# Performance work log

Measured on AMD Instinct MI355X. Metric: run time of the kernel, lower is better.

The kernel has to match this reference:

```python
import jax, jax.numpy as jnp
import numpy as np

B, S, E, H, Dh = 2, 2048, 1024, 16, 64


def setup_inputs() -> dict:
    key = jax.random.key(0)
    ks = jax.random.split(key, 8)
    w = 0.02
    return {
        "x": jax.random.normal(ks[0], (B, S, E), jnp.float32),
        # torch Linear convention: weight (out, in) = (Dh, E), stacked over heads
        "Wq": jax.random.normal(ks[1], (H, Dh, E), jnp.float32) * w,
        "bq": jax.random.normal(ks[2], (H, Dh), jnp.float32) * w,
        "Wk": jax.random.normal(ks[3], (H, Dh, E), jnp.float32) * w,
        "bk": jax.random.normal(ks[4], (H, Dh), jnp.float32) * w,
        "Wv": jax.random.normal(ks[5], (H, Dh, E), jnp.float32) * w,
        "bv": jax.random.normal(ks[6], (H, Dh), jnp.float32) * w,
        "proj": jax.random.normal(ks[7], (H * Dh, E), jnp.float32) * w,
    }


def reference(x, Wq, bq, Wk, bk, Wv, bv, proj):
    b, s, e = x.shape
    h, dh, _ = Wq.shape
    scale = jnp.sqrt(jnp.asarray(dh, x.dtype))
    # per-head linear projections: y = x @ W.T + b  -> (b, h, s, dh)
    q = jnp.einsum('bse,hde->bhsd', x, Wq) + bq[None, :, None, :]
    k = jnp.einsum('bse,hde->bhsd', x, Wk) + bk[None, :, None, :]
    v = jnp.einsum('bse,hde->bhsd', x, Wv) + bv[None, :, None, :]
    causal = jnp.triu(jnp.ones((s, s), bool), 1)
    scores = jnp.einsum('bhsd,bhtd->bhst', q, k) / scale
    scores = jnp.where(causal[None, None], -jnp.inf, scores)
    # quirk: softmax output divided by sqrt(head_size) a second time
    att = jax.nn.softmax(scores, axis=-1) / scale
    z = jnp.einsum('bhst,bhtd->bhsd', att, v)
    # quirk: torch reshapes (B,H,S,Dh) row-major into (B,S,H*Dh) WITHOUT transpose
    z = z.reshape(b, s, h * dh)
    return z @ proj
```

## Files before the change

kernel.cpp:

```cpp
#include <hip/hip_runtime.h>
#include <hip/hip_bf16.h>

typedef unsigned short u16;
typedef unsigned int u32;
typedef __bf16 bf16x8 __attribute__((ext_vector_type(8)));
typedef float f32x4 __attribute__((ext_vector_type(4)));
typedef u16 u16x8 __attribute__((ext_vector_type(8)));
typedef u16 u16x4 __attribute__((ext_vector_type(4)));
typedef u32 u32x4 __attribute__((ext_vector_type(4)));

#define B_ 2
#define S_ 2048
#define E_ 1024
#define H_ 16
#define Dh_ 64

static __device__ __forceinline__ u16 f2bf(float f) {
  unsigned u = __builtin_bit_cast(unsigned, f);
  u += 0x7fff + ((u >> 16) & 1);
  return (u16)(u >> 16);
}

static __device__ __forceinline__ void gload16(const u16* g, u16* l) {
  __builtin_amdgcn_global_load_lds((const __attribute__((address_space(1))) unsigned int*)g,
                                   (__attribute__((address_space(3))) unsigned int*)l,
                                   16, 0, 0);
}

__global__ void cvt_all(const float* __restrict__ x, const float* __restrict__ wq,
                        const float* __restrict__ wk, const float* __restrict__ wv,
                        u16* __restrict__ xb, u16* __restrict__ wcat) {
  const int i = blockIdx.x * 256 + threadIdx.x;
  const float* src; u16x8* dst;
  if (i < 524288) {
    src = x + (size_t)i * 8;            dst = (u16x8*)xb + i;
  } else {
    const int j = i - 524288;
    dst = (u16x8*)wcat + j;
    if (j < 131072)      src = wq + (size_t)j * 8;
    else if (j < 262144) src = wk + (size_t)(j - 131072) * 8;
    else                 src = wv + (size_t)(j - 262144) * 8;
  }
  float4 a = ((const float4*)src)[0], b = ((const float4*)src)[1];
  u16x8 o;
  o[0] = f2bf(a.x); o[1] = f2bf(a.y); o[2] = f2bf(a.z); o[3] = f2bf(a.w);
  o[4] = f2bf(b.x); o[5] = f2bf(b.y); o[6] = f2bf(b.z); o[7] = f2bf(b.w);
  *dst = o;
}

__global__ void transpose_cvt(const float* __restrict__ in, u16* __restrict__ outT) {
  __shared__ float t[32][33];
  const int e = blockIdx.x * 32 + threadIdx.x;
  const int f = blockIdx.y * 32 + threadIdx.y;
  t[threadIdx.y][threadIdx.x] = in[f * 1024 + e];
  __syncthreads();
  const int eo = blockIdx.x * 32 + threadIdx.y;
  const int fo = blockIdx.y * 32 + threadIdx.x;
  outT[eo * 1024 + fo] = f2bf(t[threadIdx.x][threadIdx.y]);
}

__global__ __launch_bounds__(256) void qkv_gemm(const u16* __restrict__ Wcat,
                                                const u16* __restrict__ Xm,
                                                const float* __restrict__ bq,
                                                const float* __restrict__ bk,
                                                const float* __restrict__ bv,
                                                u16* __restrict__ Qb, u16* __restrict__ Kb,
                                                u16* __restrict__ Vtb, float qs) {
  __shared__ __align__(16) u16 As[2][4096];
  __shared__ __align__(16) u16 Bs[2][4096];
  const int tid = threadIdx.x;
  const int wv = tid >> 6, ln = tid & 63;
  const int lq = ln & 15, lg = ln >> 4;
  const int bid = blockIdx.x;
  const int xcd = bid & 7, within = bid >> 3;
  const int bx = (xcd & 1) * 12 + within % 12;
  const int by = (xcd >> 1) * 8 + within / 12;
  const int ra0 = bx * 128, rb0 = by * 128;
  const int wra = wv >> 1, wrb = wv & 1;

  f32x4 acc[4][4];
  const f32x4 z4 = {0.f, 0.f, 0.f, 0.f};
#pragma unroll
  for (int i = 0; i < 4; ++i)
#pragma unroll
    for (int j = 0; j < 4; ++j) acc[i][j] = z4;

  const int arow = tid >> 2;
  const int acol = (tid & 3) * 8;
  const u16* Ags = Wcat + (ra0 + arow) * 1024 + acol;
  const u16* Bgs = Xm + (rb0 + arow) * 1024 + acol;

#define GSTAGE(KT, BUF) do { const int k0_ = (KT) * 32;              \
    gload16(Ags + k0_,         &As[BUF][wv * 512]);                  \
    gload16(Ags + 65536 + k0_, &As[BUF][wv * 512 + 2048]);           \
    gload16(Bgs + k0_,         &Bs[BUF][wv * 512]);                  \
    gload16(Bgs + 65536 + k0_, &Bs[BUF][wv * 512 + 2048]); } while (0)

  GSTAGE(0, 0);
  for (int kt = 0; kt < 32; ++kt) {
    const int cb = kt & 1;
    if (kt < 31) {
      GSTAGE(kt + 1, cb ^ 1);
      asm volatile("s_waitcnt vmcnt(4)" ::: "memory");
    } else {
      asm volatile("s_waitcnt vmcnt(0)" ::: "memory");
    }
    __builtin_amdgcn_s_barrier();
    __builtin_amdgcn_sched_barrier(0);
    bf16x8 af[4], bfr[4];
#pragma unroll
    for (int i = 0; i < 4; ++i)
      af[i] = *(const bf16x8*)&As[cb][(wra * 64 + i * 16 + lq) * 32 + lg * 8];
#pragma unroll
    for (int j = 0; j < 4; ++j)
      bfr[j] = *(const bf16x8*)&Bs[cb][(wrb * 64 + j * 16 + lq) * 32 + lg * 8];
#pragma unroll
    for (int i = 0; i < 4; ++i)
#pragma unroll
      for (int j = 0; j < 4; ++j)
        acc[i][j] = __builtin_amdgcn_mfma_f32_16x16x32_bf16(af[i], bfr[j], acc[i][j], 0, 0, 0);
    __builtin_amdgcn_sched_barrier(0);
    __builtin_amdgcn_s_barrier();
  }
#undef GSTAGE

  const int region = bx >> 3;
  const float* bias = (region == 0) ? bq : (region == 1) ? bk : bv;
  const float osc = (region == 0) ? qs : 1.0f;
  const int Ar = ra0 + wra * 64, Br = rb0 + wrb * 64;
#pragma unroll
  for (int i = 0; i < 4; ++i) {
#pragma unroll
    for (int j = 0; j < 4; ++j) {
      const int n0 = Ar + i * 16 + lg * 4;
      const int nl = n0 & 1023;
      const int h = nl >> 6, d = nl & 63;
      const int m = Br + j * 16 + lq;
      const int bb = m >> 11, s = m & 2047;
      const float4 b4 = *(const float4*)&bias[nl];
      if (region < 2) {
        u16* out = (region == 0) ? Qb : Kb;
        u16x4 pk;
        pk[0] = f2bf((acc[i][j][0] + b4.x) * osc);
        pk[1] = f2bf((acc[i][j][1] + b4.y) * osc);
        pk[2] = f2bf((acc[i][j][2] + b4.z) * osc);
        pk[3] = f2bf((acc[i][j][3] + b4.w) * osc);
        *(u16x4*)&out[((bb * H_ + h) * S_ + s) * Dh_ + d] = pk;
      } else {
        const float bvv[4] = {b4.x, b4.y, b4.z, b4.w};
#pragma unroll
        for (int r = 0; r < 4; ++r)
          Vtb[((bb * H_ + h) * Dh_ + d + r) * S_ + s] = f2bf(acc[i][j][r] + bvv[r]);
      }
    }
  }
}

__global__ __launch_bounds__(256) void proj_gemm(const u16* __restrict__ Am,
                                                 const u16* __restrict__ Bm,
                                                 float* __restrict__ out) {
  __shared__ __align__(16) u16 As[2][4096];
  __shared__ __align__(16) u16 Bs[2][2048];
  const int tid = threadIdx.x;
  const int wv = tid >> 6, ln = tid & 63;
  const int lq = ln & 15, lg = ln >> 4;
  const int bid = blockIdx.x;
  const int xcd = bid & 7, within = bid >> 3;
  const int bx = within & 7;
  const int by = xcd * 8 + (within >> 3);
  const int ra0 = bx * 128, rb0 = by * 64;
  const int wra = wv >> 1, wrb = wv & 1;

  f32x4 acc[4][2];
  const f32x4 z4 = {0.f, 0.f, 0.f, 0.f};
#pragma unroll
  for (int i = 0; i < 4; ++i)
#pragma unroll
    for (int j = 0; j < 2; ++j) acc[i][j] = z4;

  const int arow = tid >> 2;
  const int acol = (tid & 3) * 8;
  const int brow = wv * 16 + (ln >> 2);
  const int bcol = (ln & 3) * 8;
  const u16* Ags = Am + (ra0 + arow) * 1024 + acol;
  const u16* Bgs = Bm + (rb0 + brow) * 1024 + bcol;

#define PSTAGE(KT, BUF) do { const int k0_ = (KT) * 32;              \
    gload16(Ags + k0_,         &As[BUF][wv * 512]);                  \
    gload16(Ags + 65536 + k0_, &As[BUF][wv * 512 + 2048]);           \
    gload16(Bgs + k0_,         &Bs[BUF][wv * 512]); } while (0)

  PSTAGE(0, 0);
  for (int kt = 0; kt < 32; ++kt) {
    const int cb = kt & 1;
    if (kt < 31) {
      PSTAGE(kt + 1, cb ^ 1);
      asm volatile("s_waitcnt vmcnt(3)" ::: "memory");
    } else {
      asm volatile("s_waitcnt vmcnt(0)" ::: "memory");
    }
    __builtin_amdgcn_s_barrier();
    __builtin_amdgcn_sched_barrier(0);
    bf16x8 af[4], bfr[2];
#pragma unroll
    for (int i = 0; i < 4; ++i)
      af[i] = *(const bf16x8*)&As[cb][(wra * 64 + i * 16 + lq) * 32 + lg * 8];
#pragma unroll
    for (int j = 0; j < 2; ++j)
      bfr[j] = *(const bf16x8*)&Bs[cb][(wrb * 32 + j * 16 + lq) * 32 + lg * 8];
#pragma unroll
    for (int i = 0; i < 4; ++i)
#pragma unroll
      for (int j = 0; j < 2; ++j)
        acc[i][j] = __builtin_amdgcn_mfma_f32_16x16x32_bf16(af[i], bfr[j], acc[i][j], 0, 0, 0);
    __builtin_amdgcn_sched_barrier(0);
    __builtin_amdgcn_s_barrier();
  }
#undef PSTAGE

  const int Ar = ra0 + wra * 64, Br = rb0 + wrb * 32;
#pragma unroll
  for (int i = 0; i < 4; ++i)
#pragma unroll
    for (int j = 0; j < 2; ++j) {
      const int e0 = Ar + i * 16 + lg * 4;
      const int m = Br + j * 16 + lq;
      *(f32x4*)&out[m * 1024 + e0] = acc[i][j];
    }
}

__global__ __launch_bounds__(256) void attn_kernel(const u16* __restrict__ Q,
                                                   const u16* __restrict__ K,
                                                   const u16* __restrict__ Vt,
                                                   u16* __restrict__ Z) {
  __shared__ __align__(16) u16 Ktile[2][8192];
  __shared__ __align__(16) u16 Vtile[2][8192];
  const int tid = threadIdx.x;
  const int wv = tid >> 6, ln = tid & 63;
  const int lq = ln & 15, lg = ln >> 4;
  const bool lgodd = (lg & 1) != 0;
  const int id = blockIdx.x;
  const int within = id >> 3;
  const int xg = id & 7;
  int bh, qt;
  if (within < 32) { bh = xg * 4 + (within >> 4);     qt = 15 - (within & 15); }
  else { const int w = within - 32; bh = xg * 4 + 2 + (w >> 4); qt = w & 15; }
  const int qbase = (qt << 7) + wv * 32;
  const u16* Qp = Q + (size_t)bh * S_ * Dh_;
  const u16* Kp = K + (size_t)bh * S_ * Dh_;
  const u16* Vp = Vt + (size_t)bh * Dh_ * S_;

  int kgofs[4], vgrow[4], vgcol[4];
#pragma unroll
  for (int j = 0; j < 4; ++j) {
    const int p = wv * 256 + j * 64 + ln;
    const int gk = p ^ ((p >> 3) & 7);
    kgofs[j] = (gk >> 3) * 64 + (gk & 7) * 8;
    vgrow[j] = p >> 4;
    vgcol[j] = ((p & 15) ^ ((p >> 4) & 15)) * 8;
  }
  const int wv2 = wv * 2048;
  const int sc0 = (lg ^ (lq & 7)) * 8;
  const int sc1 = ((4 + lg) ^ (lq & 7)) * 8;

  bf16x8 qf[2][2];
#pragma unroll
  for (int m = 0; m < 2; ++m)
#pragma unroll
    for (int kk = 0; kk < 2; ++kk)
      qf[m][kk] = *(const bf16x8*)&Qp[(qbase + m * 16 + lq) * Dh_ + kk * 32 + lg * 8];

  f32x4 o[2][4];
  const f32x4 z4 = {0.f, 0.f, 0.f, 0.f};
#pragma unroll
  for (int m = 0; m < 2; ++m)
#pragma unroll
    for (int dt = 0; dt < 4; ++dt) o[m][dt] = z4;
  float l_lane[2] = {0.f, 0.f};

#define STAGE(KT, BUF) do { const int kb_ = (KT) * 128;                          \
    gload16(Kp + (size_t)kb_ * 64 + kgofs[0], &Ktile[BUF][wv2]);                 \
    gload16(Kp + (size_t)kb_ * 64 + kgofs[1], &Ktile[BUF][wv2 + 512]);           \
    gload16(Kp + (size_t)kb_ * 64 + kgofs[2], &Ktile[BUF][wv2 + 1024]);          \
    gload16(Kp + (size_t)kb_ * 64 + kgofs[3], &Ktile[BUF][wv2 + 1536]);          \
    gload16(Vp + (size_t)vgrow[0] * 2048 + kb_ + vgcol[0], &Vtile[BUF][wv2]);    \
    gload16(Vp + (size_t)vgrow[1] * 2048 + kb_ + vgcol[1], &Vtile[BUF][wv2 + 512]); \
    gload16(Vp + (size_t)vgrow[2] * 2048 + kb_ + vgcol[2], &Vtile[BUF][wv2 + 1024]); \
    gload16(Vp + (size_t)vgrow[3] * 2048 + kb_ + vgcol[3], &Vtile[BUF][wv2 + 1536]); \
  } while (0)

  STAGE(0, 0);
  __syncthreads();

  int cur = 0;
  for (int kt = 0; kt <= qt; ++kt) {
    if (kt < qt) STAGE(kt + 1, cur ^ 1);
    const int k0 = kt * 128;
    const bool diag = (kt == qt);
#pragma unroll
    for (int kk = 0; kk < 4; ++kk) {
      const int rA = (kk * 32 + lq) * 64;
      const int rB = rA + 1024;
      bf16x8 kA0 = *(const bf16x8*)&Ktile[cur][rA + sc0];
      bf16x8 kA1 = *(const bf16x8*)&Ktile[cur][rA + sc1];
      bf16x8 kB0 = *(const bf16x8*)&Ktile[cur][rB + sc0];
      bf16x8 kB1 = *(const bf16x8*)&Ktile[cur][rB + sc1];
      f32x4 sa0 = z4, sa1 = z4, sb0 = z4, sb1 = z4;
      __builtin_amdgcn_s_setprio(1);
      sa0 = __builtin_amdgcn_mfma_f32_16x16x32_bf16(kA0, qf[0][0], sa0, 0, 0, 0);
      sa0 = __builtin_amdgcn_mfma_f32_16x16x32_bf16(kA1, qf[0][1], sa0, 0, 0, 0);
      sa1 = __builtin_amdgcn_mfma_f32_16x16x32_bf16(kA0, qf[1][0], sa1, 0, 0, 0);
      sa1 = __builtin_amdgcn_mfma_f32_16x16x32_bf16(kA1, qf[1][1], sa1, 0, 0, 0);
      sb0 = __builtin_amdgcn_mfma_f32_16x16x32_bf16(kB0, qf[0][0], sb0, 0, 0, 0);
      sb0 = __builtin_amdgcn_mfma_f32_16x16x32_bf16(kB1, qf[0][1], sb0, 0, 0, 0);
      sb1 = __builtin_amdgcn_mfma_f32_16x16x32_bf16(kB0, qf[1][0], sb1, 0, 0, 0);
      sb1 = __builtin_amdgcn_mfma_f32_16x16x32_bf16(kB1, qf[1][1], sb1, 0, 0, 0);
      __builtin_amdgcn_s_setprio(0);
      if (diag) {
        const int keyA = k0 + kk * 32 + lg * 4;
        const int keyB = keyA + 16;
        const int qi0 = qbase + lq, qi1 = qbase + 16 + lq;
#pragma unroll
        for (int r = 0; r < 4; ++r) {
          if (keyA + r > qi0) sa0[r] = -3.0e38f;
          if (keyA + r > qi1) sa1[r] = -3.0e38f;
          if (keyB + r > qi0) sb0[r] = -3.0e38f;
          if (keyB + r > qi1) sb1[r] = -3.0e38f;
        }
      }
      u32 pA0[2], pA1[2], pB0[2], pB1[2];
#pragma unroll
      for (int m = 0; m < 2; ++m) {
        const f32x4 xa = m ? sa1 : sa0;
        const f32x4 xb = m ? sb1 : sb0;
        float e0 = __builtin_amdgcn_exp2f(xa[0]);
        float e1 = __builtin_amdgcn_exp2f(xa[1]);
        float e2 = __builtin_amdgcn_exp2f(xa[2]);
        float e3 = __builtin_amdgcn_exp2f(xa[3]);
        float f0 = __builtin_amdgcn_exp2f(xb[0]);
        float f1 = __builtin_amdgcn_exp2f(xb[1]);
        float f2 = __builtin_amdgcn_exp2f(xb[2]);
        float f3 = __builtin_amdgcn_exp2f(xb[3]);
        l_lane[m] += ((e0 + e1) + (e2 + e3)) + ((f0 + f1) + (f2 + f3));
        asm("v_cvt_pk_bf16_f32 %0, %1, %2" : "=v"(pA0[m]) : "v"(e0), "v"(e1));
        asm("v_cvt_pk_bf16_f32 %0, %1, %2" : "=v"(pA1[m]) : "v"(e2), "v"(e3));
        asm("v_cvt_pk_bf16_f32 %0, %1, %2" : "=v"(pB0[m]) : "v"(f0), "v"(f1));
        asm("v_cvt_pk_bf16_f32 %0, %1, %2" : "=v"(pB1[m]) : "v"(f2), "v"(f3));
      }
      bf16x8 pf[2];
#pragma unroll
      for (int m = 0; m < 2; ++m) {
        u32 A0 = pA0[m], B0 = pB0[m], A1 = pA1[m], B1 = pB1[m];
        asm("v_permlane32_swap_b32 %0, %1" : "+v"(A0), "+v"(B0));
        asm("v_permlane32_swap_b32 %0, %1" : "+v"(A1), "+v"(B1));
        const u32 A0x = __shfl_xor((int)A0, 16), B0x = __shfl_xor((int)B0, 16);
        const u32 A1x = __shfl_xor((int)A1, 16), B1x = __shfl_xor((int)B1, 16);
        u32x4 w;
        w[0] = lgodd ? B0x : A0;
        w[1] = lgodd ? B1x : A1;
        w[2] = lgodd ? B0 : A0x;
        w[3] = lgodd ? B1 : A1x;
        pf[m] = __builtin_bit_cast(bf16x8, w);
      }
      const int scvk = ((kk * 4 + lg) ^ lq) * 8;
      __builtin_amdgcn_s_setprio(1);
#pragma unroll
      for (int dt = 0; dt < 4; ++dt) {
        bf16x8 vf = *(const bf16x8*)&Vtile[cur][(dt * 16 + lq) * 128 + scvk];
        o[0][dt] = __builtin_amdgcn_mfma_f32_16x16x32_bf16(vf, pf[0], o[0][dt], 0, 0, 0);
        o[1][dt] = __builtin_amdgcn_mfma_f32_16x16x32_bf16(vf, pf[1], o[1][dt], 0, 0, 0);
      }
      __builtin_amdgcn_s_setprio(0);
    }
    if (kt < qt) {
      __syncthreads();
      cur ^= 1;
    }
  }
#undef STAGE

#pragma unroll
  for (int m = 0; m < 2; ++m) {
    float l = l_lane[m];
    l += __shfl_xor(l, 16);
    l += __shfl_xor(l, 32);
    const float inv = 0.125f / l;
    const int q_idx = qbase + m * 16 + lq;
#pragma unroll
    for (int dt = 0; dt < 4; ++dt) {
      u16x4 pko;
#pragma unroll
      for (int r = 0; r < 4; ++r) pko[r] = f2bf(o[m][dt][r] * inv);
      *(u16x4*)&Z[((size_t)bh * S_ + q_idx) * Dh_ + dt * 16 + lg * 4] = pko;
    }
  }
}

extern "C" void kernel_launch(void* const* d_in, const int* in_sizes, int n_in,
                              void* d_out, int out_size, void* d_ws, size_t ws_size,
                              hipStream_t stream) {
  const float* x    = (const float*)d_in[0];
  const float* Wq   = (const float*)d_in[1];
  const float* bq   = (const float*)d_in[2];
  const float* Wk   = (const float*)d_in[3];
  const float* bk   = (const float*)d_in[4];
  const float* Wv   = (const float*)d_in[5];
  const float* bv   = (const float*)d_in[6];
  const float* proj = (const float*)d_in[7];
  float* out = (float*)d_out;

  char* p = (char*)d_ws;
  u16* xb   = (u16*)p; p += (size_t)4096 * 1024 * 2;
  u16* wcat = (u16*)p; p += (size_t)3072 * 1024 * 2;
  u16* pjt  = (u16*)p; p += (size_t)1024 * 1024 * 2;
  u16* Qb   = (u16*)p; p += (size_t)4096 * 1024 * 2;
  u16* Kb   = (u16*)p; p += (size_t)4096 * 1024 * 2;
  u16* Vtb  = (u16*)p; p += (size_t)4096 * 1024 * 2;
  u16* Zb   = (u16*)p; p += (size_t)4096 * 1024 * 2;

  cvt_all<<<dim3(3584), dim3(256), 0, stream>>>(x, Wq, Wk, Wv, xb, wcat);
  transpose_cvt<<<dim3(32, 32), dim3(32, 32), 0, stream>>>(proj, pjt);

  const float qs = 0.125f * 1.44269504f;
  qkv_gemm<<<dim3(768), dim3(256), 0, stream>>>(wcat, xb, bq, bk, bv, Qb, Kb, Vtb, qs);

  attn_kernel<<<dim3(512), dim3(256), 0, stream>>>(Qb, Kb, Vtb, Zb);

  proj_gemm<<<dim3(512), dim3(256), 0, stream>>>(pjt, Zb, out);
}
```

Baseline: 113.6 us.

## Halve attention tiles, skip masked diagonal chunks, triple-buffer GEMM pipelines

The attention kernel now uses 64-query by 64-key tiles with 16 queries per wave, and launches twice as many blocks. On the diagonal tile it skips key chunks that are fully masked for a wave. The aim is better load balance and occupancy, plus less wasted causal work. Both GEMMs move from double to triple buffering of their LDS stages, prefetching two k-tiles ahead to hide more load latency. The trade-off is more LDS per GEMM block and more K/V reloads per query in attention, since each block now covers fewer queries.

```diff
diff --git a/kernel.cpp b/kernel.cpp
--- a/kernel.cpp
+++ b/kernel.cpp
@@ -66,8 +66,8 @@
                                                 const float* __restrict__ bv,
                                                 u16* __restrict__ Qb, u16* __restrict__ Kb,
                                                 u16* __restrict__ Vtb, float qs) {
-  __shared__ __align__(16) u16 As[2][4096];
-  __shared__ __align__(16) u16 Bs[2][4096];
+  __shared__ __align__(16) u16 As[3][4096];
+  __shared__ __align__(16) u16 Bs[3][4096];
   const int tid = threadIdx.x;
   const int wv = tid >> 6, ln = tid & 63;
   const int lq = ln & 15, lg = ln >> 4;
@@ -97,10 +97,13 @@
     gload16(Bgs + 65536 + k0_, &Bs[BUF][wv * 512 + 2048]); } while (0)
 
   GSTAGE(0, 0);
+  GSTAGE(1, 1);
   for (int kt = 0; kt < 32; ++kt) {
-    const int cb = kt & 1;
-    if (kt < 31) {
-      GSTAGE(kt + 1, cb ^ 1);
+    const int cb = kt % 3;
+    if (kt < 30) {
+      GSTAGE(kt + 2, (kt + 2) % 3);
+      asm volatile("s_waitcnt vmcnt(8)" ::: "memory");
+    } else if (kt == 30) {
       asm volatile("s_waitcnt vmcnt(4)" ::: "memory");
     } else {
       asm volatile("s_waitcnt vmcnt(0)" ::: "memory");
@@ -159,8 +162,8 @@
 __global__ __launch_bounds__(256) void proj_gemm(const u16* __restrict__ Am,
                                                  const u16* __restrict__ Bm,
                                                  float* __restrict__ out) {
-  __shared__ __align__(16) u16 As[2][4096];
-  __shared__ __align__(16) u16 Bs[2][2048];
+  __shared__ __align__(16) u16 As[3][4096];
+  __shared__ __align__(16) u16 Bs[3][2048];
   const int tid = threadIdx.x;
   const int wv = tid >> 6, ln = tid & 63;
   const int lq = ln & 15, lg = ln >> 4;
@@ -191,10 +194,13 @@
     gload16(Bgs + k0_,         &Bs[BUF][wv * 512]); } while (0)
 
   PSTAGE(0, 0);
+  PSTAGE(1, 1);
   for (int kt = 0; kt < 32; ++kt) {
-    const int cb = kt & 1;
-    if (kt < 31) {
-      PSTAGE(kt + 1, cb ^ 1);
+    const int cb = kt % 3;
+    if (kt < 30) {
+      PSTAGE(kt + 2, (kt + 2) % 3);
+      asm volatile("s_waitcnt vmcnt(6)" ::: "memory");
+    } else if (kt == 30) {
       asm volatile("s_waitcnt vmcnt(3)" ::: "memory");
     } else {
       asm volatile("s_waitcnt vmcnt(0)" ::: "memory");
@@ -233,60 +239,48 @@
                                                    const u16* __restrict__ K,
                                                    const u16* __restrict__ Vt,
                                                    u16* __restrict__ Z) {
-  __shared__ __align__(16) u16 Ktile[2][8192];
-  __shared__ __align__(16) u16 Vtile[2][8192];
+  __shared__ __align__(16) u16 Ktile[2][4096];
+  __shared__ __align__(16) u16 Vtile[2][4096];
   const int tid = threadIdx.x;
   const int wv = tid >> 6, ln = tid & 63;
   const int lq = ln & 15, lg = ln >> 4;
   const bool lgodd = (lg & 1) != 0;
   const int id = blockIdx.x;
+  const int xg = id & 7;
   const int within = id >> 3;
-  const int xg = id & 7;
-  int bh, qt;
-  if (within < 32) { bh = xg * 4 + (within >> 4);     qt = 15 - (within & 15); }
-  else { const int w = within - 32; bh = xg * 4 + 2 + (w >> 4); qt = w & 15; }
-  const int qbase = (qt << 7) + wv * 32;
+  const int grp = within >> 5;
+  const int w2 = within & 31;
+  const int bh = xg * 4 + grp;
+  const int qt = (grp & 1) ? w2 : (31 - w2);
+  const int qbase = qt * 64 + wv * 16;
+  const int q_idx = qbase + lq;
   const u16* Qp = Q + (size_t)bh * S_ * Dh_;
   const u16* Kp = K + (size_t)bh * S_ * Dh_;
   const u16* Vp = Vt + (size_t)bh * Dh_ * S_;
 
-  int kgofs[4], vgrow[4], vgcol[4];
-#pragma unroll
-  for (int j = 0; j < 4; ++j) {
-    const int p = wv * 256 + j * 64 + ln;
-    const int gk = p ^ ((p >> 3) & 7);
-    kgofs[j] = (gk >> 3) * 64 + (gk & 7) * 8;
-    vgrow[j] = p >> 4;
-    vgcol[j] = ((p & 15) ^ ((p >> 4) & 15)) * 8;
-  }
-  const int wv2 = wv * 2048;
+  const int p0 = wv * 128 + ln, p1 = p0 + 64;
+  const int g0 = p0 ^ ((p0 >> 3) & 7), g1 = p1 ^ ((p1 >> 3) & 7);
+  const int gr0 = g0 >> 3, gc0 = (g0 & 7) * 8;
+  const int gr1 = g1 >> 3, gc1 = (g1 & 7) * 8;
+  const int lb0 = wv * 1024, lb1 = wv * 1024 + 512;
   const int sc0 = (lg ^ (lq & 7)) * 8;
   const int sc1 = ((4 + lg) ^ (lq & 7)) * 8;
 
-  bf16x8 qf[2][2];
-#pragma unroll
-  for (int m = 0; m < 2; ++m)
-#pragma unroll
-    for (int kk = 0; kk < 2; ++kk)
-      qf[m][kk] = *(const bf16x8*)&Qp[(qbase + m * 16 + lq) * Dh_ + kk * 32 + lg * 8];
-
-  f32x4 o[2][4];
+  bf16x8 qf[2];
+  qf[0] = *(const bf16x8*)&Qp[q_idx * Dh_ + lg * 8];
+  qf[1] = *(const bf16x8*)&Qp[q_idx * Dh_ + 32 + lg * 8];
+
+  f32x4 o[4];
   const f32x4 z4 = {0.f, 0.f, 0.f, 0.f};
 #pragma unroll
-  for (int m = 0; m < 2; ++m)
-#pragma unroll
-    for (int dt = 0; dt < 4; ++dt) o[m][dt] = z4;
-  float l_lane[2] = {0.f, 0.f};
-
-#define STAGE(KT, BUF) do { const int kb_ = (KT) * 128;                          \
-    gload16(Kp + (size_t)kb_ * 64 + kgofs[0], &Ktile[BUF][wv2]);                 \
-    gload16(Kp + (size_t)kb_ * 64 + kgofs[1], &Ktile[BUF][wv2 + 512]);           \
-    gload16(Kp + (size_t)kb_ * 64 + kgofs[2], &Ktile[BUF][wv2 + 1024]);          \
-    gload16(Kp + (size_t)kb_ * 64 + kgofs[3], &Ktile[BUF][wv2 + 1536]);          \
-    gload16(Vp + (size_t)vgrow[0] * 2048 + kb_ + vgcol[0], &Vtile[BUF][wv2]);    \
-    gload16(Vp + (size_t)vgrow[1] * 2048 + kb_ + vgcol[1], &Vtile[BUF][wv2 + 512]); \
-    gload16(Vp + (size_t)vgrow[2] * 2048 + kb_ + vgcol[2], &Vtile[BUF][wv2 + 1024]); \
-    gload16(Vp + (size_t)vgrow[3] * 2048 + kb_ + vgcol[3], &Vtile[BUF][wv2 + 1536]); \
+  for (int dt = 0; dt < 4; ++dt) o[dt] = z4;
+  float l_lane = 0.f;
+
+#define STAGE(KT, BUF) do { const int kb_ = (KT) * 64;                       \
+    gload16(Kp + (size_t)(kb_ + gr0) * 64 + gc0, &Ktile[BUF][lb0]);          \
+    gload16(Kp + (size_t)(kb_ + gr1) * 64 + gc1, &Ktile[BUF][lb1]);          \
+    gload16(Vp + (size_t)gr0 * 2048 + kb_ + gc0, &Vtile[BUF][lb0]);          \
+    gload16(Vp + (size_t)gr1 * 2048 + kb_ + gc1, &Vtile[BUF][lb1]);          \
   } while (0)
 
   STAGE(0, 0);
@@ -295,62 +289,48 @@
   int cur = 0;
   for (int kt = 0; kt <= qt; ++kt) {
     if (kt < qt) STAGE(kt + 1, cur ^ 1);
-    const int k0 = kt * 128;
+    const int k0 = kt * 64;
     const bool diag = (kt == qt);
-#pragma unroll
-    for (int kk = 0; kk < 4; ++kk) {
-      const int rA = (kk * 32 + lq) * 64;
-      const int rB = rA + 1024;
-      bf16x8 kA0 = *(const bf16x8*)&Ktile[cur][rA + sc0];
-      bf16x8 kA1 = *(const bf16x8*)&Ktile[cur][rA + sc1];
-      bf16x8 kB0 = *(const bf16x8*)&Ktile[cur][rB + sc0];
-      bf16x8 kB1 = *(const bf16x8*)&Ktile[cur][rB + sc1];
-      f32x4 sa0 = z4, sa1 = z4, sb0 = z4, sb1 = z4;
-      __builtin_amdgcn_s_setprio(1);
-      sa0 = __builtin_amdgcn_mfma_f32_16x16x32_bf16(kA0, qf[0][0], sa0, 0, 0, 0);
-      sa0 = __builtin_amdgcn_mfma_f32_16x16x32_bf16(kA1, qf[0][1], sa0, 0, 0, 0);
-      sa1 = __builtin_amdgcn_mfma_f32_16x16x32_bf16(kA0, qf[1][0], sa1, 0, 0, 0);
-      sa1 = __builtin_amdgcn_mfma_f32_16x16x32_bf16(kA1, qf[1][1], sa1, 0, 0, 0);
-      sb0 = __builtin_amdgcn_mfma_f32_16x16x32_bf16(kB0, qf[0][0], sb0, 0, 0, 0);
-      sb0 = __builtin_amdgcn_mfma_f32_16x16x32_bf16(kB1, qf[0][1], sb0, 0, 0, 0);
-      sb1 = __builtin_amdgcn_mfma_f32_16x16x32_bf16(kB0, qf[1][0], sb1, 0, 0, 0);
-      sb1 = __builtin_amdgcn_mfma_f32_16x16x32_bf16(kB1, qf[1][1], sb1, 0, 0, 0);
-      __builtin_amdgcn_s_setprio(0);
-      if (diag) {
-        const int keyA = k0 + kk * 32 + lg * 4;
-        const int keyB = keyA + 16;
-        const int qi0 = qbase + lq, qi1 = qbase + 16 + lq;
-#pragma unroll
-        for (int r = 0; r < 4; ++r) {
-          if (keyA + r > qi0) sa0[r] = -3.0e38f;
-          if (keyA + r > qi1) sa1[r] = -3.0e38f;
-          if (keyB + r > qi0) sb0[r] = -3.0e38f;
-          if (keyB + r > qi1) sb1[r] = -3.0e38f;
+    const int nkk = diag ? ((wv >> 1) + 1) : 2;
+#pragma unroll
+    for (int kk = 0; kk < 2; ++kk) {
+      if (kk < nkk) {
+        const int rA = (kk * 32 + lq) * 64;
+        const int rB = rA + 1024;
+        bf16x8 kA0 = *(const bf16x8*)&Ktile[cur][rA + sc0];
+        bf16x8 kA1 = *(const bf16x8*)&Ktile[cur][rA + sc1];
+        bf16x8 kB0 = *(const bf16x8*)&Ktile[cur][rB + sc0];
+        bf16x8 kB1 = *(const bf16x8*)&Ktile[cur][rB + sc1];
+        f32x4 sa = z4, sb = z4;
+        __builtin_amdgcn_s_setprio(1);
+        sa = __builtin_amdgcn_mfma_f32_16x16x32_bf16(kA0, qf[0], sa, 0, 0, 0);
+        sa = __builtin_amdgcn_mfma_f32_16x16x32_bf16(kA1, qf[1], sa, 0, 0, 0);
+        sb = __builtin_amdgcn_mfma_f32_16x16x32_bf16(kB0, qf[0], sb, 0, 0, 0);
+        sb = __builtin_amdgcn_mfma_f32_16x16x32_bf16(kB1, qf[1], sb, 0, 0, 0);
+        __builtin_amdgcn_s_setprio(0);
+        if (diag) {
+          const int keyA = k0 + kk * 32 + lg * 4;
+          const int keyB = keyA + 16;
+#pragma unroll
+          for (int r = 0; r < 4; ++r) {
+            if (keyA + r > q_idx) sa[r] = -3.0e38f;
+            if (keyB + r > q_idx) sb[r] = -3.0e38f;
+          }
         }
-      }
-      u32 pA0[2], pA1[2], pB0[2], pB1[2];
-#pragma unroll
-      for (int m = 0; m < 2; ++m) {
-        const f32x4 xa = m ? sa1 : sa0;
-        const f32x4 xb = m ? sb1 : sb0;
-        float e0 = __builtin_amdgcn_exp2f(xa[0]);
-        float e1 = __builtin_amdgcn_exp2f(xa[1]);
-        float e2 = __builtin_amdgcn_exp2f(xa[2]);
-        float e3 = __builtin_amdgcn_exp2f(xa[3]);
-        float f0 = __builtin_amdgcn_exp2f(xb[0]);
-        float f1 = __builtin_amdgcn_exp2f(xb[1]);
-        float f2 = __builtin_amdgcn_exp2f(xb[2]);
-        float f3 = __builtin_amdgcn_exp2f(xb[3]);
-        l_lane[m] += ((e0 + e1) + (e2 + e3)) + ((f0 + f1) + (f2 + f3));
-        asm("v_cvt_pk_bf16_f32 %0, %1, %2" : "=v"(pA0[m]) : "v"(e0), "v"(e1));
-        asm("v_cvt_pk_bf16_f32 %0, %1, %2" : "=v"(pA1[m]) : "v"(e2), "v"(e3));
-        asm("v_cvt_pk_bf16_f32 %0, %1, %2" : "=v"(pB0[m]) : "v"(f0), "v"(f1));
-        asm("v_cvt_pk_bf16_f32 %0, %1, %2" : "=v"(pB1[m]) : "v"(f2), "v"(f3));
-      }
-      bf16x8 pf[2];
-#pragma unroll
-      for (int m = 0; m < 2; ++m) {
-        u32 A0 = pA0[m], B0 = pB0[m], A1 = pA1[m], B1 = pB1[m];
+        float e0 = __builtin_amdgcn_exp2f(sa[0]);
+        float e1 = __builtin_amdgcn_exp2f(sa[1]);
+        float e2 = __builtin_amdgcn_exp2f(sa[2]);
+        float e3 = __builtin_amdgcn_exp2f(sa[3]);
+        float f0 = __builtin_amdgcn_exp2f(sb[0]);
+        float f1 = __builtin_amdgcn_exp2f(sb[1]);
+        float f2 = __builtin_amdgcn_exp2f(sb[2]);
+        float f3 = __builtin_amdgcn_exp2f(sb[3]);
+        l_lane += ((e0 + e1) + (e2 + e3)) + ((f0 + f1) + (f2 + f3));
+        u32 A0, A1, B0, B1;
+        asm("v_cvt_pk_bf16_f32 %0, %1, %2" : "=v"(A0) : "v"(e0), "v"(e1));
+        asm("v_cvt_pk_bf16_f32 %0, %1, %2" : "=v"(A1) : "v"(e2), "v"(e3));
+        asm("v_cvt_pk_bf16_f32 %0, %1, %2" : "=v"(B0) : "v"(f0), "v"(f1));
+        asm("v_cvt_pk_bf16_f32 %0, %1, %2" : "=v"(B1) : "v"(f2), "v"(f3));
         asm("v_permlane32_swap_b32 %0, %1" : "+v"(A0), "+v"(B0));
         asm("v_permlane32_swap_b32 %0, %1" : "+v"(A1), "+v"(B1));
         const u32 A0x = __shfl_xor((int)A0, 16), B0x = __shfl_xor((int)B0, 16);
@@ -360,17 +340,16 @@
         w[1] = lgodd ? B1x : A1;
         w[2] = lgodd ? B0 : A0x;
         w[3] = lgodd ? B1 : A1x;
-        pf[m] = __builtin_bit_cast(bf16x8, w);
+        const bf16x8 pf = __builtin_bit_cast(bf16x8, w);
+        const int scvk = ((kk * 4 + lg) ^ (lq & 7)) * 8;
+        __builtin_amdgcn_s_setprio(1);
+#pragma unroll
+        for (int dt = 0; dt < 4; ++dt) {
+          bf16x8 vf = *(const bf16x8*)&Vtile[cur][(dt * 16 + lq) * 64 + scvk];
+          o[dt] = __builtin_amdgcn_mfma_f32_16x16x32_bf16(vf, pf, o[dt], 0, 0, 0);
+        }
+        __builtin_amdgcn_s_setprio(0);
       }
-      const int scvk = ((kk * 4 + lg) ^ lq) * 8;
-      __builtin_amdgcn_s_setprio(1);
-#pragma unroll
-      for (int dt = 0; dt < 4; ++dt) {
-        bf16x8 vf = *(const bf16x8*)&Vtile[cur][(dt * 16 + lq) * 128 + scvk];
-        o[0][dt] = __builtin_amdgcn_mfma_f32_16x16x32_bf16(vf, pf[0], o[0][dt], 0, 0, 0);
-        o[1][dt] = __builtin_amdgcn_mfma_f32_16x16x32_bf16(vf, pf[1], o[1][dt], 0, 0, 0);
-      }
-      __builtin_amdgcn_s_setprio(0);
     }
     if (kt < qt) {
       __syncthreads();
@@ -379,20 +358,16 @@
   }
 #undef STAGE
 
-#pragma unroll
-  for (int m = 0; m < 2; ++m) {
-    float l = l_lane[m];
-    l += __shfl_xor(l, 16);
-    l += __shfl_xor(l, 32);
-    const float inv = 0.125f / l;
-    const int q_idx = qbase + m * 16 + lq;
-#pragma unroll
-    for (int dt = 0; dt < 4; ++dt) {
-      u16x4 pko;
-#pragma unroll
-      for (int r = 0; r < 4; ++r) pko[r] = f2bf(o[m][dt][r] * inv);
-      *(u16x4*)&Z[((size_t)bh * S_ + q_idx) * Dh_ + dt * 16 + lg * 4] = pko;
-    }
+  float l = l_lane;
+  l += __shfl_xor(l, 16);
+  l += __shfl_xor(l, 32);
+  const float inv = 0.125f / l;
+#pragma unroll
+  for (int dt = 0; dt < 4; ++dt) {
+    u16x4 pko;
+#pragma unroll
+    for (int r = 0; r < 4; ++r) pko[r] = f2bf(o[dt][r] * inv);
+    *(u16x4*)&Z[((size_t)bh * S_ + q_idx) * Dh_ + dt * 16 + lg * 4] = pko;
   }
 }
 
@@ -424,7 +399,7 @@
   const float qs = 0.125f * 1.44269504f;
   qkv_gemm<<<dim3(768), dim3(256), 0, stream>>>(wcat, xb, bq, bk, bv, Qb, Kb, Vtb, qs);
 
-  attn_kernel<<<dim3(512), dim3(256), 0, stream>>>(Qb, Kb, Vtb, Zb);
+  attn_kernel<<<dim3(1024), dim3(256), 0, stream>>>(Qb, Kb, Vtb, Zb);
 
   proj_gemm<<<dim3(512), dim3(256), 0, stream>>>(pjt, Zb, out);
 }
```

After: 128.7 us. 1.13x slower.
